# Optimization experiments

Measured on AMD Instinct MI355X. Metric: run time of the kernel, lower is better.

## Reference

```python
import jax, jax.numpy as jnp
import numpy as np

P = 81        # provinces (sequence length)
E = 256       # H_ENC_COLS, encoder feature width per province
H = 4096      # stand-in for ORDER_VOCABULARY_SIZE (LSTMCell units)


def setup_inputs() -> dict:
    key = jax.random.key(0)
    k0, k1, k2, k3 = jax.random.split(key, 4)
    h_enc = jax.random.normal(k0, (P, E), dtype=jnp.float32)
    h0 = jax.random.normal(k1, (H,), dtype=jnp.float32) * 0.1  # tf.random.normal stddev=0.1
    W = jax.random.normal(k2, (E + H, 4 * H), dtype=jnp.float32) * 0.02  # input kernel
    U = jax.random.normal(k3, (H, 4 * H), dtype=jnp.float32) * 0.02      # recurrent kernel
    b = jnp.zeros((4 * H,), dtype=jnp.float32)
    return {"h_enc": h_enc, "h0": h0, "W": W, "U": U, "b": b}


def reference(h_enc, h0, W, U, b):
    # Keras LSTMCell(units=H, activation=None): gate order i,f,c,o;
    # recurrent_activation=sigmoid, candidate/output activation = identity.
    Hd = h0.shape[0]

    def step(carry, x_t):
        h, c = carry
        x = jnp.concatenate([x_t, h])            # [E+H] concat(province, h_dec)
        z = x @ W + h @ U + b                    # [4H]
        i, f, g, o = jnp.split(z, 4)
        i = jax.nn.sigmoid(i)
        f = jax.nn.sigmoid(f)
        o = jax.nn.sigmoid(o)
        c_new = f * c + i * g                    # activation=None -> linear candidate
        h_new = o * c_new                        # activation=None -> linear output
        return (h_new, c_new), h                 # emit pre-update h (= valid_orders)

    c0 = jnp.zeros((Hd,), dtype=h0.dtype)
    (_, _), orders = jax.lax.scan(step, (h0, c0), h_enc)
    return orders  # [P, H]
```

## Files before the change

kernel.cpp:

```cpp
#include <hip/hip_runtime.h>
#include <hip/hip_fp16.h>
#include <cstddef>

#define Pn 81
#define En 256
#define Hn 4096
#define H4 16384
#define KSPLIT 64
#define KC (Hn / KSPLIT)
#define CG 8
#define TT 16

__device__ __forceinline__ size_t mt_slice(int kc, int cg) {
    return ((size_t)(kc * CG + cg)) * (KC * 256);
}

__global__ __launch_bounds__(256) void xproj_kernel(const float* __restrict__ henc,
                                                    const float* __restrict__ W,
                                                    const float* __restrict__ bias,
                                                    float* __restrict__ X) {
    int col = blockIdx.x * 256 + threadIdx.x;
    int t0  = blockIdx.y * TT;
    __shared__ float hs[TT][En];
    for (int r = threadIdx.x; r < TT * En; r += 256) {
        int tt = r >> 8;
        int e  = r & (En - 1);
        hs[tt][e] = (t0 + tt < Pn) ? henc[(size_t)(t0 + tt) * En + e] : 0.f;
    }
    __syncthreads();
    float acc[TT];
    float bc = bias[col];
#pragma unroll
    for (int tt = 0; tt < TT; ++tt) acc[tt] = bc;
    for (int e = 0; e < En; ++e) {
        float w = W[(size_t)e * H4 + col];
#pragma unroll
        for (int tt = 0; tt < TT; ++tt) acc[tt] += hs[tt][e] * w;
    }
    int nt = Pn - t0; if (nt > TT) nt = TT;
    for (int tt = 0; tt < nt; ++tt) X[(size_t)(t0 + tt) * H4 + col] = acc[tt];
}

__global__ __launch_bounds__(256) void init_kernel(const float* __restrict__ h0,
                                                   float* __restrict__ orders,
                                                   float* __restrict__ c0) {
    int i = blockIdx.x * 256 + threadIdx.x;
    orders[i] = h0[i];
    c0[i] = 0.f;
}

__global__ __launch_bounds__(512) void fuse_step0_kernel(const float* __restrict__ W,
                                                         const float* __restrict__ U,
                                                         const float* __restrict__ h0,
                                                         __half* __restrict__ Mt,
                                                         float* __restrict__ zcur) {
    const int cg  = blockIdx.x;
    const int kc  = blockIdx.y;
    const int tid = threadIdx.x;
    __shared__ float hs[KC];
    if (tid < KC) hs[tid] = h0[kc * KC + tid];
    __syncthreads();

    const int half = tid >> 8;
    const int t256 = tid & 255;
    const int c0   = cg * 2048 + t256 * 8;
    uint4* M8 = (uint4*)Mt;
    const size_t slice = mt_slice(kc, cg);

    float acc[8];
#pragma unroll
    for (int p = 0; p < 8; ++p) acc[p] = 0.f;

#pragma unroll 4
    for (int k = 0; k < 32; ++k) {
        const int krow = kc * KC + half * 32 + k;
        const float4* Wp = (const float4*)(W + (size_t)(En + krow) * H4 + c0);
        const float4* Up = (const float4*)(U + (size_t)krow * H4 + c0);
        float4 w0 = Wp[0], w1 = Wp[1];
        float4 u0 = Up[0], u1 = Up[1];
        float m[8];
        m[0] = w0.x + u0.x; m[1] = w0.y + u0.y; m[2] = w0.z + u0.z; m[3] = w0.w + u0.w;
        m[4] = w1.x + u1.x; m[5] = w1.y + u1.y; m[6] = w1.z + u1.z; m[7] = w1.w + u1.w;
        alignas(16) __half hm[8];
#pragma unroll
        for (int p = 0; p < 8; ++p) hm[p] = __float2half(m[p]);
        M8[slice + (size_t)(half * 32 + k) * 256 + t256] = *(const uint4*)hm;
        float hk = hs[half * 32 + k];
#pragma unroll
        for (int p = 0; p < 8; ++p) acc[p] += hk * m[p];
    }

    __shared__ float accbuf[256][9];
    if (half == 1) {
#pragma unroll
        for (int p = 0; p < 8; ++p) accbuf[t256][p] = acc[p];
    }
    __syncthreads();
    if (half == 0) {
#pragma unroll
        for (int p = 0; p < 8; ++p) acc[p] += accbuf[t256][p];
        float4* zp = (float4*)(zcur + (size_t)kc * H4 + (size_t)c0);
        zp[0] = make_float4(acc[0], acc[1], acc[2], acc[3]);
        zp[1] = make_float4(acc[4], acc[5], acc[6], acc[7]);
    }
}

__global__ __launch_bounds__(512) void step_kernel(const __half* __restrict__ Mt,
                                                   const float* __restrict__ X,
                                                   const float* __restrict__ zprev,
                                                   float* __restrict__ zcur,
                                                   const float* __restrict__ cprev,
                                                   float* __restrict__ ccur,
                                                   float* __restrict__ orders,
                                                   int t) {
    const int cg  = blockIdx.x;
    const int kc  = blockIdx.y;
    const int tid = threadIdx.x;
    const int half = tid >> 8;
    const int t256 = tid & 255;
    const uint4* M8 = (const uint4*)Mt;
    const size_t slice = mt_slice(kc, cg);

    uint4 buf[8];
#pragma unroll
    for (int p = 0; p < 8; ++p) buf[p] = M8[slice + (size_t)p * 512 + tid];

    __shared__ float hs[KC];
    {
        const int lane = tid & 63;
        const int g    = tid >> 6;
        const int j    = kc * KC + lane;
        float s0 = 0.f, s1 = 0.f, s2 = 0.f, s3 = 0.f;
        for (int ks = g; ks < KSPLIT; ks += 8) {
            const float* zp = zprev + (size_t)ks * H4;
            s0 += zp[j];
            s1 += zp[j + Hn];
            s2 += zp[j + 2 * Hn];
            s3 += zp[j + 3 * Hn];
        }
        __shared__ float red[4][8][64];
        red[0][g][lane] = s0;
        red[1][g][lane] = s1;
        red[2][g][lane] = s2;
        red[3][g][lane] = s3;
        __syncthreads();
        if (g == 0) {
            const float* Xt = X + (size_t)(t - 1) * H4;
            float zi = Xt[j], zf = Xt[j + Hn], zg = Xt[j + 2 * Hn], zo = Xt[j + 3 * Hn];
#pragma unroll
            for (int g2 = 0; g2 < 8; ++g2) {
                zi += red[0][g2][lane];
                zf += red[1][g2][lane];
                zg += red[2][g2][lane];
                zo += red[3][g2][lane];
            }
            float gi = 1.f / (1.f + __expf(-zi));
            float gf = 1.f / (1.f + __expf(-zf));
            float go = 1.f / (1.f + __expf(-zo));
            float cn = gf * cprev[j] + gi * zg;
            float hn = go * cn;
            orders[(size_t)t * Hn + j] = hn;
            ccur[j] = cn;
            hs[lane] = hn;
        }
    }
    __syncthreads();

    float acc[8];
#pragma unroll
    for (int p = 0; p < 8; ++p) acc[p] = 0.f;
#pragma unroll
    for (int kb = 0; kb < 32; kb += 8) {
#pragma unroll
        for (int p = 0; p < 8; ++p) {
            uint4 raw = buf[p];
            int kn = kb + p + 8;
            if (kn < 32) buf[p] = M8[slice + (size_t)kn * 512 + tid];
            float hk = hs[2 * (kb + p) + half];
            const __half2* hp = (const __half2*)&raw;
#pragma unroll
            for (int q = 0; q < 4; ++q) {
                float2 f = __half22float2(hp[q]);
                acc[2 * q]     += hk * f.x;
                acc[2 * q + 1] += hk * f.y;
            }
        }
    }

    __shared__ float accbuf[256][9];
    if (half == 1) {
#pragma unroll
        for (int p = 0; p < 8; ++p) accbuf[t256][p] = acc[p];
    }
    __syncthreads();
    if (half == 0) {
#pragma unroll
        for (int p = 0; p < 8; ++p) acc[p] += accbuf[t256][p];
        float4* zp = (float4*)(zcur + (size_t)kc * H4 + (size_t)(cg * 256 + t256) * 8);
        zp[0] = make_float4(acc[0], acc[1], acc[2], acc[3]);
        zp[1] = make_float4(acc[4], acc[5], acc[6], acc[7]);
    }
}

__global__ __launch_bounds__(256) void final_gate_kernel(const float* __restrict__ zprev,
                                                         const float* __restrict__ X,
                                                         const float* __restrict__ cprev,
                                                         float* __restrict__ orders) {
    const int lane = threadIdx.x & 63;
    const int g    = threadIdx.x >> 6;
    const int j    = blockIdx.x * 64 + lane;
    float s0 = 0.f, s1 = 0.f, s2 = 0.f, s3 = 0.f;
    for (int ks = g; ks < KSPLIT; ks += 4) {
        const float* zp = zprev + (size_t)ks * H4;
        s0 += zp[j];
        s1 += zp[j + Hn];
        s2 += zp[j + 2 * Hn];
        s3 += zp[j + 3 * Hn];
    }
    __shared__ float red[4][4][64];
    red[0][g][lane] = s0;
    red[1][g][lane] = s1;
    red[2][g][lane] = s2;
    red[3][g][lane] = s3;
    __syncthreads();
    if (g == 0) {
        const float* Xt = X + (size_t)(Pn - 2) * H4;
        float zi = Xt[j]          + red[0][0][lane] + red[0][1][lane] + red[0][2][lane] + red[0][3][lane];
        float zf = Xt[j + Hn]     + red[1][0][lane] + red[1][1][lane] + red[1][2][lane] + red[1][3][lane];
        float zg = Xt[j + 2 * Hn] + red[2][0][lane] + red[2][1][lane] + red[2][2][lane] + red[2][3][lane];
        float zo = Xt[j + 3 * Hn] + red[3][0][lane] + red[3][1][lane] + red[3][2][lane] + red[3][3][lane];
        float gi = 1.f / (1.f + __expf(-zi));
        float gf = 1.f / (1.f + __expf(-zf));
        float go = 1.f / (1.f + __expf(-zo));
        float cn = gf * cprev[j] + gi * zg;
        orders[(size_t)(Pn - 1) * Hn + j] = go * cn;
    }
}

__global__ __launch_bounds__(256) void fb_init_kernel(const float* __restrict__ h0,
                                                      float* __restrict__ h,
                                                      float* __restrict__ c) {
    int i = blockIdx.x * 256 + threadIdx.x;
    h[i] = h0[i];
    c[i] = 0.f;
}

__global__ __launch_bounds__(256) void matvec2_kernel(const float* __restrict__ Wh,
                                                      const float* __restrict__ U,
                                                      const float* __restrict__ h,
                                                      float* __restrict__ zpart) {
    int col4 = blockIdx.x * 256 + threadIdx.x;
    int k0   = blockIdx.y * KC;
    __shared__ float hs[KC];
    if (threadIdx.x < KC) hs[threadIdx.x] = h[k0 + threadIdx.x];
    __syncthreads();
    const float4* W4 = (const float4*)Wh;
    const float4* U4 = (const float4*)U;
    size_t base = (size_t)k0 * (H4 / 4) + col4;
    float4 acc; acc.x = acc.y = acc.z = acc.w = 0.f;
#pragma unroll 2
    for (int k = 0; k < KC; ++k) {
        size_t idx = base + (size_t)k * (H4 / 4);
        float4 w = W4[idx];
        float4 u = U4[idx];
        float hk = hs[k];
        acc.x += hk * (w.x + u.x); acc.y += hk * (w.y + u.y);
        acc.z += hk * (w.z + u.z); acc.w += hk * (w.w + u.w);
    }
    ((float4*)zpart)[(size_t)blockIdx.y * (H4 / 4) + col4] = acc;
}

__global__ __launch_bounds__(256) void gate_kernel(const float* __restrict__ zpart,
                                                   const float* __restrict__ X,
                                                   float* __restrict__ h,
                                                   float* __restrict__ c,
                                                   float* __restrict__ orders,
                                                   int t) {
    int lane = threadIdx.x & 63;
    int g    = threadIdx.x >> 6;
    int j    = blockIdx.x * 64 + lane;
    float s0 = 0.f, s1 = 0.f, s2 = 0.f, s3 = 0.f;
    for (int ks = g; ks < KSPLIT; ks += 4) {
        const float* zp = zpart + (size_t)ks * H4;
        s0 += zp[j];
        s1 += zp[j + Hn];
        s2 += zp[j + 2 * Hn];
        s3 += zp[j + 3 * Hn];
    }
    __shared__ float red[4][4][64];
    red[0][g][lane] = s0;
    red[1][g][lane] = s1;
    red[2][g][lane] = s2;
    red[3][g][lane] = s3;
    __syncthreads();
    if (g == 0) {
        const float* Xt = X + (size_t)t * H4;
        float zi = Xt[j]          + red[0][0][lane] + red[0][1][lane] + red[0][2][lane] + red[0][3][lane];
        float zf = Xt[j + Hn]     + red[1][0][lane] + red[1][1][lane] + red[1][2][lane] + red[1][3][lane];
        float zg = Xt[j + 2 * Hn] + red[2][0][lane] + red[2][1][lane] + red[2][2][lane] + red[2][3][lane];
        float zo = Xt[j + 3 * Hn] + red[3][0][lane] + red[3][1][lane] + red[3][2][lane] + red[3][3][lane];
        float gi = 1.f / (1.f + __expf(-zi));
        float gf = 1.f / (1.f + __expf(-zf));
        float go = 1.f / (1.f + __expf(-zo));
        float cn = gf * c[j] + gi * zg;
        float ho = h[j];
        float hn = go * cn;
        orders[(size_t)t * Hn + j] = ho;
        h[j] = hn;
        c[j] = cn;
    }
}

extern "C" void kernel_launch(void* const* d_in, const int* in_sizes, int n_in,
                              void* d_out, int out_size, void* d_ws, size_t ws_size,
                              hipStream_t stream) {
    const float* henc = (const float*)d_in[0];
    const float* h0   = (const float*)d_in[1];
    const float* W    = (const float*)d_in[2];
    const float* U    = (const float*)d_in[3];
    const float* bias = (const float*)d_in[4];
    float* out = (float*)d_out;

    const size_t needM = (size_t)Hn * H4 * sizeof(__half);
    const size_t needX = (size_t)Pn * H4 * sizeof(float);
    const size_t needZ = (size_t)KSPLIT * H4 * sizeof(float);
    const size_t needC = (size_t)Hn * sizeof(float);

    char* ws = (char*)d_ws;
    const bool fused = ws_size >= needM + needX + 2 * needZ + 2 * needC;

    if (fused) {
        __half* Mt = (__half*)ws;
        float*  X  = (float*)(ws + needM);
        float*  zp[2];
        zp[0] = (float*)(ws + needM + needX);
        zp[1] = (float*)(ws + needM + needX + needZ);
        float* cb[2];
        cb[0] = (float*)(ws + needM + needX + 2 * needZ);
        cb[1] = cb[0] + Hn;

        xproj_kernel<<<dim3(H4 / 256, (Pn + TT - 1) / TT), 256, 0, stream>>>(henc, W, bias, X);
        init_kernel<<<dim3(Hn / 256), 256, 0, stream>>>(h0, out, cb[0]);
        fuse_step0_kernel<<<dim3(CG, KSPLIT), 512, 0, stream>>>(W, U, h0, Mt, zp[0]);

        for (int t = 1; t < Pn - 1; ++t) {
            step_kernel<<<dim3(CG, KSPLIT), 512, 0, stream>>>(
                Mt, X, zp[(t + 1) & 1], zp[t & 1],
                cb[(t + 1) & 1], cb[t & 1], out, t);
        }
        final_gate_kernel<<<dim3(Hn / 64), 256, 0, stream>>>(zp[1], X, cb[1], out);
    } else {
        float* X     = (float*)ws;
        float* zpart = (float*)(ws + needX);
        float* h     = (float*)(ws + needX + needZ);
        float* c     = h + Hn;

        xproj_kernel<<<dim3(H4 / 256, (Pn + TT - 1) / TT), 256, 0, stream>>>(henc, W, bias, X);
        fb_init_kernel<<<dim3(Hn / 256), 256, 0, stream>>>(h0, h, c);
        for (int t = 0; t < Pn; ++t) {
            matvec2_kernel<<<dim3(H4 / 4 / 256, KSPLIT), 256, 0, stream>>>(
                W + (size_t)En * H4, U, h, zpart);
            gate_kernel<<<dim3(Hn / 64), 256, 0, stream>>>(zpart, X, h, c, out, t);
        }
    }
}
```

Baseline: 2.464 ms.

## Halve K-split, use 1024-thread step blocks, and separate fp16 weight conversion

Cuts KSPLIT from 64 to 32 so each step block handles 128 k-rows with 1024 threads split across four quarters, which halves the partial-sum buffer each step must reduce. The fused step0 kernel becomes a pure convert kernel spread over more blocks, and step 0 now runs through the regular step kernel using h0. Only the cgp==0 block writes orders and c. In exchange the grid has half as many blocks, blocks are larger, and prefetching is simplified to just the first 8 rows.

Measured after the change: 2.030 ms. -17.6%, faster.

```diff
diff --git a/kernel.cpp b/kernel.cpp
--- a/kernel.cpp
+++ b/kernel.cpp
@@ -6,13 +6,13 @@
 #define En 256
 #define Hn 4096
 #define H4 16384
-#define KSPLIT 64
+#define KSPLIT 32
 #define KC (Hn / KSPLIT)
 #define CG 8
 #define TT 16
 
-__device__ __forceinline__ size_t mt_slice(int kc, int cg) {
-    return ((size_t)(kc * CG + cg)) * (KC * 256);
+__device__ __forceinline__ size_t mt_slice(int kc, int cgp) {
+    return ((size_t)(kc * CG + cgp)) * ((size_t)KC * 256);
 }
 
 __global__ __launch_bounds__(256) void xproj_kernel(const float* __restrict__ henc,
@@ -49,96 +49,72 @@
     c0[i] = 0.f;
 }
 
-__global__ __launch_bounds__(512) void fuse_step0_kernel(const float* __restrict__ W,
-                                                         const float* __restrict__ U,
-                                                         const float* __restrict__ h0,
-                                                         __half* __restrict__ Mt,
-                                                         float* __restrict__ zcur) {
-    const int cg  = blockIdx.x;
+__global__ __launch_bounds__(256) void fuse_convert_kernel(const float* __restrict__ W,
+                                                           const float* __restrict__ U,
+                                                           __half* __restrict__ Mt) {
+    const int q   = blockIdx.x & 7;
+    const int cgp = blockIdx.x >> 3;
     const int kc  = blockIdx.y;
     const int tid = threadIdx.x;
-    __shared__ float hs[KC];
-    if (tid < KC) hs[tid] = h0[kc * KC + tid];
-    __syncthreads();
-
-    const int half = tid >> 8;
-    const int t256 = tid & 255;
-    const int c0   = cg * 2048 + t256 * 8;
+    const int c0  = cgp * 2048 + tid * 8;
     uint4* M8 = (uint4*)Mt;
-    const size_t slice = mt_slice(kc, cg);
-
-    float acc[8];
-#pragma unroll
-    for (int p = 0; p < 8; ++p) acc[p] = 0.f;
-
+    const size_t slice = mt_slice(kc, cgp);
 #pragma unroll 4
-    for (int k = 0; k < 32; ++k) {
-        const int krow = kc * KC + half * 32 + k;
+    for (int k = 0; k < 16; ++k) {
+        const int kl   = q * 16 + k;
+        const int krow = kc * KC + kl;
         const float4* Wp = (const float4*)(W + (size_t)(En + krow) * H4 + c0);
         const float4* Up = (const float4*)(U + (size_t)krow * H4 + c0);
         float4 w0 = Wp[0], w1 = Wp[1];
         float4 u0 = Up[0], u1 = Up[1];
-        float m[8];
-        m[0] = w0.x + u0.x; m[1] = w0.y + u0.y; m[2] = w0.z + u0.z; m[3] = w0.w + u0.w;
-        m[4] = w1.x + u1.x; m[5] = w1.y + u1.y; m[6] = w1.z + u1.z; m[7] = w1.w + u1.w;
-        alignas(16) __half hm[8];
-#pragma unroll
-        for (int p = 0; p < 8; ++p) hm[p] = __float2half(m[p]);
-        M8[slice + (size_t)(half * 32 + k) * 256 + t256] = *(const uint4*)hm;
-        float hk = hs[half * 32 + k];
-#pragma unroll
-        for (int p = 0; p < 8; ++p) acc[p] += hk * m[p];
-    }
-
-    __shared__ float accbuf[256][9];
-    if (half == 1) {
-#pragma unroll
-        for (int p = 0; p < 8; ++p) accbuf[t256][p] = acc[p];
-    }
-    __syncthreads();
-    if (half == 0) {
-#pragma unroll
-        for (int p = 0; p < 8; ++p) acc[p] += accbuf[t256][p];
-        float4* zp = (float4*)(zcur + (size_t)kc * H4 + (size_t)c0);
-        zp[0] = make_float4(acc[0], acc[1], acc[2], acc[3]);
-        zp[1] = make_float4(acc[4], acc[5], acc[6], acc[7]);
-    }
-}
-
-__global__ __launch_bounds__(512) void step_kernel(const __half* __restrict__ Mt,
-                                                   const float* __restrict__ X,
-                                                   const float* __restrict__ zprev,
-                                                   float* __restrict__ zcur,
-                                                   const float* __restrict__ cprev,
-                                                   float* __restrict__ ccur,
-                                                   float* __restrict__ orders,
-                                                   int t) {
-    const int cg  = blockIdx.x;
-    const int kc  = blockIdx.y;
-    const int tid = threadIdx.x;
+        alignas(16) __half2 hm[4];
+        hm[0] = __floats2half2_rn(w0.x + u0.x, w0.y + u0.y);
+        hm[1] = __floats2half2_rn(w0.z + u0.z, w0.w + u0.w);
+        hm[2] = __floats2half2_rn(w1.x + u1.x, w1.y + u1.y);
+        hm[3] = __floats2half2_rn(w1.z + u1.z, w1.w + u1.w);
+        M8[slice + (size_t)kl * 256 + tid] = *(const uint4*)hm;
+    }
+}
+
+__global__ __launch_bounds__(1024) void step_kernel(const __half* __restrict__ Mt,
+                                                    const float* __restrict__ X,
+                                                    const float* __restrict__ zprev,
+                                                    float* __restrict__ zcur,
+                                                    const float* __restrict__ cprev,
+                                                    float* __restrict__ ccur,
+                                                    float* __restrict__ orders,
+                                                    const float* __restrict__ h0,
+                                                    int t) {
+    const int cgp  = blockIdx.x;
+    const int kc   = blockIdx.y;
+    const int tid  = threadIdx.x;
     const int half = tid >> 8;
     const int t256 = tid & 255;
     const uint4* M8 = (const uint4*)Mt;
-    const size_t slice = mt_slice(kc, cg);
+    const size_t slice = mt_slice(kc, cgp);
 
     uint4 buf[8];
 #pragma unroll
-    for (int p = 0; p < 8; ++p) buf[p] = M8[slice + (size_t)p * 512 + tid];
+    for (int p = 0; p < 8; ++p)
+        buf[p] = M8[slice + (size_t)(half * 32 + p) * 256 + t256];
 
     __shared__ float hs[KC];
-    {
-        const int lane = tid & 63;
-        const int g    = tid >> 6;
+    if (t == 0) {
+        if (tid < KC) hs[tid] = h0[kc * KC + tid];
+    } else {
+        const int lane = tid & 127;
+        const int g    = tid >> 7;
         const int j    = kc * KC + lane;
         float s0 = 0.f, s1 = 0.f, s2 = 0.f, s3 = 0.f;
+#pragma unroll
         for (int ks = g; ks < KSPLIT; ks += 8) {
-            const float* zp = zprev + (size_t)ks * H4;
-            s0 += zp[j];
-            s1 += zp[j + Hn];
-            s2 += zp[j + 2 * Hn];
-            s3 += zp[j + 3 * Hn];
-        }
-        __shared__ float red[4][8][64];
+            const float* zpp = zprev + (size_t)ks * H4;
+            s0 += zpp[j];
+            s1 += zpp[j + Hn];
+            s2 += zpp[j + 2 * Hn];
+            s3 += zpp[j + 3 * Hn];
+        }
+        __shared__ float red[4][8][KC];
         red[0][g][lane] = s0;
         red[1][g][lane] = s1;
         red[2][g][lane] = s2;
@@ -159,8 +135,10 @@
             float go = 1.f / (1.f + __expf(-zo));
             float cn = gf * cprev[j] + gi * zg;
             float hn = go * cn;
-            orders[(size_t)t * Hn + j] = hn;
-            ccur[j] = cn;
+            if (cgp == 0) {
+                orders[(size_t)t * Hn + j] = hn;
+                ccur[j] = cn;
+            }
             hs[lane] = hn;
         }
     }
@@ -170,35 +148,32 @@
 #pragma unroll
     for (int p = 0; p < 8; ++p) acc[p] = 0.f;
 #pragma unroll
-    for (int kb = 0; kb < 32; kb += 8) {
-#pragma unroll
-        for (int p = 0; p < 8; ++p) {
-            uint4 raw = buf[p];
-            int kn = kb + p + 8;
-            if (kn < 32) buf[p] = M8[slice + (size_t)kn * 512 + tid];
-            float hk = hs[2 * (kb + p) + half];
-            const __half2* hp = (const __half2*)&raw;
-#pragma unroll
-            for (int q = 0; q < 4; ++q) {
-                float2 f = __half22float2(hp[q]);
-                acc[2 * q]     += hk * f.x;
-                acc[2 * q + 1] += hk * f.y;
-            }
-        }
-    }
-
-    __shared__ float accbuf[256][9];
-    if (half == 1) {
-#pragma unroll
-        for (int p = 0; p < 8; ++p) accbuf[t256][p] = acc[p];
+    for (int k = 0; k < 32; ++k) {
+        uint4 raw;
+        if (k < 8) raw = buf[k];
+        else       raw = M8[slice + (size_t)(half * 32 + k) * 256 + t256];
+        float hk = hs[half * 32 + k];
+        const __half2* hp = (const __half2*)&raw;
+#pragma unroll
+        for (int q = 0; q < 4; ++q) {
+            float2 f = __half22float2(hp[q]);
+            acc[2 * q]     += hk * f.x;
+            acc[2 * q + 1] += hk * f.y;
+        }
+    }
+    __shared__ float accbuf[3][256][9];
+    if (half != 0) {
+#pragma unroll
+        for (int p = 0; p < 8; ++p) accbuf[half - 1][t256][p] = acc[p];
     }
     __syncthreads();
     if (half == 0) {
 #pragma unroll
-        for (int p = 0; p < 8; ++p) acc[p] += accbuf[t256][p];
-        float4* zp = (float4*)(zcur + (size_t)kc * H4 + (size_t)(cg * 256 + t256) * 8);
-        zp[0] = make_float4(acc[0], acc[1], acc[2], acc[3]);
-        zp[1] = make_float4(acc[4], acc[5], acc[6], acc[7]);
+        for (int p = 0; p < 8; ++p)
+            acc[p] += accbuf[0][t256][p] + accbuf[1][t256][p] + accbuf[2][t256][p];
+        float4* zw = (float4*)(zcur + (size_t)kc * H4 + (size_t)(cgp * 256 + t256) * 8);
+        zw[0] = make_float4(acc[0], acc[1], acc[2], acc[3]);
+        zw[1] = make_float4(acc[4], acc[5], acc[6], acc[7]);
     }
 }
 
@@ -210,6 +185,7 @@
     const int g    = threadIdx.x >> 6;
     const int j    = blockIdx.x * 64 + lane;
     float s0 = 0.f, s1 = 0.f, s2 = 0.f, s3 = 0.f;
+#pragma unroll
     for (int ks = g; ks < KSPLIT; ks += 4) {
         const float* zp = zprev + (size_t)ks * H4;
         s0 += zp[j];
@@ -280,6 +256,7 @@
     int g    = threadIdx.x >> 6;
     int j    = blockIdx.x * 64 + lane;
     float s0 = 0.f, s1 = 0.f, s2 = 0.f, s3 = 0.f;
+#pragma unroll
     for (int ks = g; ks < KSPLIT; ks += 4) {
         const float* zp = zpart + (size_t)ks * H4;
         s0 += zp[j];
@@ -330,23 +307,23 @@
     const bool fused = ws_size >= needM + needX + 2 * needZ + 2 * needC;
 
     if (fused) {
-        __half* Mt = (__half*)ws;
-        float*  X  = (float*)(ws + needM);
-        float*  zp[2];
-        zp[0] = (float*)(ws + needM + needX);
-        zp[1] = (float*)(ws + needM + needX + needZ);
-        float* cb[2];
-        cb[0] = (float*)(ws + needM + needX + 2 * needZ);
-        cb[1] = cb[0] + Hn;
+        __half* Mt  = (__half*)ws;
+        float*  X   = (float*)(ws + needM);
+        float*  z0  = (float*)(ws + needM + needX);
+        float*  z1  = (float*)(ws + needM + needX + needZ);
+        float*  cb0 = (float*)(ws + needM + needX + 2 * needZ);
+        float*  cb1 = cb0 + Hn;
 
         xproj_kernel<<<dim3(H4 / 256, (Pn + TT - 1) / TT), 256, 0, stream>>>(henc, W, bias, X);
-        init_kernel<<<dim3(Hn / 256), 256, 0, stream>>>(h0, out, cb[0]);
-        fuse_step0_kernel<<<dim3(CG, KSPLIT), 512, 0, stream>>>(W, U, h0, Mt, zp[0]);
-
-        for (int t = 1; t < Pn - 1; ++t) {
-            step_kernel<<<dim3(CG, KSPLIT), 512, 0, stream>>>(
+        init_kernel<<<dim3(Hn / 256), 256, 0, stream>>>(h0, out, cb0);
+        fuse_convert_kernel<<<dim3(CG * 8, KSPLIT), 256, 0, stream>>>(W, U, Mt);
+
+        float* zp[2] = {z0, z1};
+        float* cb[2] = {cb0, cb1};
+        for (int t = 0; t < Pn - 1; ++t) {
+            step_kernel<<<dim3(CG, KSPLIT), 1024, 0, stream>>>(
                 Mt, X, zp[(t + 1) & 1], zp[t & 1],
-                cb[(t + 1) & 1], cb[t & 1], out, t);
+                cb[(t + 1) & 1], cb[t & 1], out, h0, t);
         }
         final_gate_kernel<<<dim3(Hn / 64), 256, 0, stream>>>(zp[1], X, cb[1], out);
     } else {
```
